# Kernel tuning notes

Hardware: AMD Instinct MI355X
Metric: run time of the kernel (lower is better)

## Reference

```python
import jax, jax.numpy as jnp
import numpy as np

B, LC, LX, LH = 2048, 20, 20, 200
D, H, V, DENSE = 128, 512, 100000, 256
MAXSEQ = 200


def _ln(x, g, b, eps=1e-5):
    m = jnp.mean(x, axis=-1, keepdims=True)
    v = jnp.mean((x - m) ** 2, axis=-1, keepdims=True)
    return (x - m) * jax.lax.rsqrt(v + eps) * g + b


def _masked_mean(x, mask):
    # x: [B,L,D], mask: [B,L] (0/1)
    m = mask.astype(x.dtype)[..., None]
    s = jnp.sum(x * m, axis=1)
    cnt = jnp.clip(jnp.sum(m, axis=1), 1.0, None)
    return s / cnt


def setup_inputs() -> dict:
    key = jax.random.key(0)
    ks = jax.random.split(key, 40)
    s = 0.02
    rn = lambda k, shape: jax.random.normal(k, shape, dtype=jnp.float32) * s
    tok_emb = rn(ks[10], (V, D)).at[0].set(0.0)          # padding_idx=0
    grp_emb = rn(ks[12], (4, D)).at[0].set(0.0)          # padding_idx=0
    return {
        'candidate_tokens': jax.random.randint(ks[0], (B, LC), 0, V),
        'context_tokens': jax.random.randint(ks[1], (B, LX), 0, V),
        'history_tokens': jax.random.randint(ks[2], (B, LH), 0, V),
        'history_positions': jax.random.randint(ks[3], (B, LH), 0, MAXSEQ + 1),
        'history_groups': jax.random.randint(ks[4], (B, LH), 0, 4),
        'candidate_mask': jax.random.randint(ks[5], (B, LC), 0, 2),
        'context_mask': jax.random.randint(ks[6], (B, LX), 0, 2),
        'history_mask': jax.random.randint(ks[7], (B, LH), 0, 2),
        'history_times': jax.random.uniform(ks[8], (B, LH), dtype=jnp.float32),
        'dense_features': jax.random.normal(ks[9], (B, DENSE), dtype=jnp.float32),
        'tok_emb': tok_emb,
        'pos_emb': rn(ks[11], (MAXSEQ + 1, D)),
        'grp_emb': grp_emb,
        'time_w1': rn(ks[13], (1, D)), 'time_b1': jnp.zeros((D,)),
        'time_w2': rn(ks[14], (D, D)), 'time_b2': jnp.zeros((D,)),
        'comp_w': rn(ks[15], (2 * D, D)), 'comp_b': jnp.zeros((D,)),
        'comp_g': jnp.ones((D,)), 'comp_bt': jnp.zeros((D,)),
        'dense_w': rn(ks[16], (DENSE, H)), 'dense_b': jnp.zeros((H,)),
        'dense_g': jnp.ones((H,)), 'dense_bt': jnp.zeros((H,)),
        'query_w': rn(ks[17], (3 * D + H, D)), 'query_b': jnp.zeros((D,)),
        'query_g': jnp.ones((D,)), 'query_bt': jnp.zeros((D,)),
        'out_w1': rn(ks[18], (7 * D + H, H)), 'out_b1': jnp.zeros((H,)),
        'out_g': jnp.ones((H,)), 'out_bt': jnp.zeros((H,)),
        'out_w2': rn(ks[19], (H, H // 2)), 'out_b2': jnp.zeros((H // 2,)),
        'out_w3': rn(ks[20], (H // 2, 1)), 'out_b3': jnp.zeros((1,)),
    }


def reference(candidate_tokens, context_tokens, history_tokens, history_positions,
              history_groups, candidate_mask, context_mask, history_mask,
              history_times, dense_features,
              tok_emb, pos_emb, grp_emb,
              time_w1, time_b1, time_w2, time_b2,
              comp_w, comp_b, comp_g, comp_bt,
              dense_w, dense_b, dense_g, dense_bt,
              query_w, query_b, query_g, query_bt,
              out_w1, out_b1, out_g, out_bt,
              out_w2, out_b2, out_w3, out_b3):
    silu = jax.nn.silu
    cand_e = tok_emb[candidate_tokens]          # [B,LC,D]
    ctx_e = tok_emb[context_tokens]             # [B,LX,D]
    tok_h = tok_emb[history_tokens]             # [B,LH,D]
    pos_h = pos_emb[history_positions]
    grp_h = grp_emb[history_groups]
    t = history_times[..., None]                # [B,LH,1]
    time_h = silu(t @ time_w1 + time_b1) @ time_w2 + time_b2
    history_embeddings = tok_h + pos_h + grp_h + time_h
    comp_in = jnp.concatenate([grp_h, time_h], axis=-1)  # [B,LH,2D]
    component_summary = silu(_ln(comp_in @ comp_w + comp_b, comp_g, comp_bt))
    cand_s = _masked_mean(cand_e, candidate_mask)
    ctx_s = _masked_mean(ctx_e, context_mask)
    comp_hist_s = _masked_mean(component_summary, history_mask)
    dense_s = silu(_ln(dense_features @ dense_w + dense_b, dense_g, dense_bt))
    q_in = jnp.concatenate([cand_s, ctx_s, comp_hist_s, dense_s], axis=-1)
    query = silu(_ln(q_in @ query_w + query_b, query_g, query_bt))  # [B,D]
    # masked attention pooling
    scores = jnp.einsum('bld,bd->bl', history_embeddings, query) / jnp.sqrt(jnp.float32(D))
    scores = jnp.where(history_mask > 0, scores, -1e9)
    attn = jax.nn.softmax(scores, axis=-1)
    hist_s = jnp.einsum('bl,bld->bd', attn, history_embeddings)
    interaction = cand_s * hist_s
    comp_inter = cand_s * comp_hist_s
    diff = jnp.abs(hist_s - comp_hist_s)
    fused = jnp.concatenate([cand_s, ctx_s, hist_s, comp_hist_s,
                             interaction, comp_inter, diff, dense_s], axis=-1)
    h1 = silu(_ln(fused @ out_w1 + out_b1, out_g, out_bt))
    h2 = silu(h1 @ out_w2 + out_b2)
    return (h2 @ out_w3 + out_b3).squeeze(-1)   # [B]
```

## Files before the change

kernel.cpp:

```cpp
#include <hip/hip_runtime.h>
#include <hip/hip_bf16.h>

#define B_ 2048
#define LC_ 20
#define LX_ 20
#define LH_ 200
#define D_ 128
#define H_ 512
#define DENSE_ 256

typedef __attribute__((ext_vector_type(8))) short short8v;
typedef __attribute__((ext_vector_type(4))) short short4v;
typedef __attribute__((ext_vector_type(4))) float floatx4;

__device__ __forceinline__ float siluf(float x) { return x / (1.f + __expf(-x)); }

__device__ __forceinline__ unsigned short f2bf(float f) {
  return __builtin_bit_cast(unsigned short, __float2bfloat16(f));
}
__device__ __forceinline__ float bf2f(unsigned short u) {
  return __bfloat162float(__builtin_bit_cast(__hip_bfloat16, u));
}

__device__ __forceinline__ float wredsum(float v) {
#pragma unroll
  for (int off = 32; off > 0; off >>= 1) v += __shfl_xor(v, off, 64);
  return v;
}

__device__ __forceinline__ int cidx(int a, int b) {
  if (a > b) { int t = a; a = b; b = t; }
  const int base[5] = {0, 5, 9, 12, 14};
  return base[a] + (b - a);
}

__global__ __launch_bounds__(128) void k0a_E(
    const float* __restrict__ w1, const float* __restrict__ b1,
    const float* __restrict__ W2, const float* __restrict__ b2,
    float* __restrict__ E) {
  __shared__ float sc[128];
  int j = threadIdx.x, p = blockIdx.x;
  {
    float w = w1[j], bb = b1[j];
    float y0 = siluf(bb);
    float y1 = siluf(0.25f * w + bb);
    float y2 = siluf(0.50f * w + bb);
    float y3 = siluf(0.75f * w + bb);
    float y4 = siluf(w + bb);
    float d1 = y1 - y0;
    float d2 = y2 - 2.f * y1 + y0;
    float d3 = y3 - 3.f * y2 + 3.f * y1 - y0;
    float d4 = y4 - 4.f * y3 + 6.f * y2 - 4.f * y1 + y0;
    float c0 = y0;
    float c1 = d1 - 0.5f * d2 + d3 * (1.f / 3.f) - 0.25f * d4;
    float c2 = 0.5f * d2 - 0.5f * d3 + (11.f / 24.f) * d4;
    float c3 = d3 * (1.f / 6.f) - 0.25f * d4;
    float c4 = d4 * (1.f / 24.f);
    float cp;
    if (p == 0) cp = c0;
    else if (p == 1) cp = c1 * 4.f;
    else if (p == 2) cp = c2 * 16.f;
    else if (p == 3) cp = c3 * 64.f;
    else cp = c4 * 256.f;
    sc[j] = cp;
  }
  __syncthreads();
  float acc = 0.f;
#pragma unroll 8
  for (int kk = 0; kk < 128; ++kk) acc += sc[kk] * W2[kk * 128 + j];
  if (p == 0) acc += b2[j];
  E[p * 128 + j] = acc;
}

__global__ __launch_bounds__(128) void k0b_FG(
    const float* __restrict__ E, const float* __restrict__ grp_emb,
    const float* __restrict__ comp_w, const float* __restrict__ comp_b,
    float* __restrict__ F, float* __restrict__ gvec) {
  __shared__ float sv[128];
  int j = threadIdx.x, blk = blockIdx.x;
  if (blk < 5) {
    sv[j] = E[blk * 128 + j];
    __syncthreads();
    float acc = 0.f;
#pragma unroll 8
    for (int kk = 0; kk < 128; ++kk) acc += sv[kk] * comp_w[(128 + kk) * 128 + j];
    if (blk == 0) acc += comp_b[j];
    F[blk * 128 + j] = acc;
  } else {
    int g = blk - 5;
    sv[j] = grp_emb[g * 128 + j];
    __syncthreads();
    float acc = 0.f;
#pragma unroll 8
    for (int kk = 0; kk < 128; ++kk) acc += sv[kk] * comp_w[kk * 128 + j];
    gvec[g * 128 + j] = acc;
  }
}

__global__ __launch_bounds__(512) void k0c_fit(
    const float* __restrict__ F, const float* __restrict__ gvec,
    const float* __restrict__ cg_, const float* __restrict__ cbt_,
    float* __restrict__ CC) {
  __shared__ float sF2[640];
  __shared__ float sGv[512];
  __shared__ float s48[48];
  __shared__ float sMC[20], sVC[36];
  int tid = threadIdx.x;
  for (int idx = tid; idx < 640; idx += 512) sF2[idx] = F[idx];
  if (tid < 512) sGv[tid] = gvec[tid];
  __syncthreads();
  int wv = tid >> 6, lane = tid & 63;
#pragma unroll
  for (int i = 0; i < 6; ++i) {
    int m = wv * 6 + i;
    if (m < 48) {
      const float* va;
      const float* vb = nullptr;
      int t = m;
      if (t < 5) va = &sF2[t * 128];
      else if (t < 9) va = &sGv[(t - 5) * 128];
      else if (t < 13) { va = &sGv[(t - 9) * 128]; vb = va; }
      else if (t < 33) {
        int g = (t - 13) / 5, p = (t - 13) % 5;
        va = &sGv[g * 128]; vb = &sF2[p * 128];
      } else {
        int idx = t - 33;
        int a = 0;
        if (idx >= 14) a = 4;
        else if (idx >= 12) a = 3;
        else if (idx >= 9) a = 2;
        else if (idx >= 5) a = 1;
        const int base[5] = {0, 5, 9, 12, 14};
        int bcol = a + (idx - base[a]);
        va = &sF2[a * 128]; vb = &sF2[bcol * 128];
      }
      float s;
      if (vb) s = va[lane] * vb[lane] + va[lane + 64] * vb[lane + 64];
      else    s = va[lane] + va[lane + 64];
      s = wredsum(s);
      if (lane == 0) s48[m] = s * (1.f / 128.f);
    }
  }
  __syncthreads();
  if (tid < 20) {
    int g = tid / 5, p = tid % 5;
    sMC[g * 5 + p] = s48[p] + (p == 0 ? s48[5 + g] : 0.f);
  }
  if (tid < 36) {
    int g = tid / 9, kk = tid % 9;
    float v = (kk == 0 ? s48[9 + g] : 0.f);
    if (kk < 5) v += 2.f * s48[13 + g * 5 + kk];
#pragma unroll
    for (int p = 0; p < 5; ++p) {
      int q = kk - p;
      if (q >= 0 && q <= 4) v += s48[33 + cidx(p, q)];
    }
    sVC[g * 9 + kk] = v;
  }
  __syncthreads();
  const float nodes[11] = {0.f, 0.02447174185f, 0.09549150281f, 0.2061073739f,
                           0.3454915028f, 0.5f, 0.6545084972f, 0.7938926261f,
                           0.9045084972f, 0.9755282581f, 1.f};
  int g = tid >> 7, j = tid & 127;
  float cgj = cg_[j], btj = cbt_[j];
  float F0 = sF2[j], F1 = sF2[128 + j], F2v = sF2[256 + j], F3 = sF2[384 + j], F4 = sF2[512 + j];
  const float* mc = &sMC[g * 5];
  const float* vc = &sVC[g * 9];
  float gv = sGv[g * 128 + j];
  float fv[11];
#pragma unroll
  for (int n = 0; n < 11; ++n) {
    float t = nodes[n];
    float mean = (((mc[4] * t + mc[3]) * t + mc[2]) * t + mc[1]) * t + mc[0];
    float e2 = vc[8];
#pragma unroll
    for (int p = 7; p >= 0; --p) e2 = e2 * t + vc[p];
    float rstd = rsqrtf(e2 - mean * mean + 1e-5f);
    float pre = gv + ((((F4 * t + F3) * t + F2v) * t + F1) * t + F0);
    fv[n] = siluf((pre - mean) * rstd * cgj + btj);
  }
#pragma unroll
  for (int ord = 1; ord <= 10; ++ord) {
#pragma unroll
    for (int n = 10; n >= 1; --n) {
      if (n >= ord) fv[n] = (fv[n] - fv[n - 1]) / (nodes[n] - nodes[n - ord]);
    }
  }
  float c[11];
#pragma unroll
  for (int i = 0; i < 11; ++i) c[i] = 0.f;
  c[0] = fv[10];
#pragma unroll
  for (int n = 9; n >= 0; --n) {
    int deg = 9 - n;
    float x = nodes[n];
    c[deg + 1] = c[deg];
#pragma unroll
    for (int i = 10; i >= 1; --i) {
      if (i <= deg) c[i] = c[i - 1] - x * c[i];
    }
    c[0] = fv[n] - x * c[0];
  }
#pragma unroll
  for (int p = 0; p < 11; ++p) CC[(g * 11 + p) * 128 + j] = c[p];
}

__global__ __launch_bounds__(256) void k_convw1t(
    const float* __restrict__ ow1, unsigned short* __restrict__ BT) {
  __shared__ float tile[64][65];
  int bk = blockIdx.x % 22;
  int bn = blockIdx.x / 22;
  int tx = threadIdx.x & 63, ty = threadIdx.x >> 6;
#pragma unroll
  for (int r = 0; r < 16; ++r) {
    int kl = ty * 16 + r;
    tile[kl][tx] = ow1[(size_t)(bk * 64 + kl) * 512 + bn * 64 + tx];
  }
  __syncthreads();
#pragma unroll
  for (int r = 0; r < 16; ++r) {
    int nl = ty * 16 + r;
    BT[(size_t)(bn * 64 + nl) * 1408 + bk * 64 + tx] = f2bf(tile[tx][nl]);
  }
}

__global__ __launch_bounds__(256) void k_convmisc(
    const float* __restrict__ ow2, const float* __restrict__ qw,
    const float* __restrict__ dw, const float* __restrict__ df,
    unsigned short* __restrict__ OW2BT, unsigned short* __restrict__ QWBT,
    unsigned short* __restrict__ DWBT, unsigned short* __restrict__ DB) {
  int idx = blockIdx.x * 256 + threadIdx.x;
  if (idx < 131072) {
    int n = idx >> 9, k = idx & 511;
    OW2BT[(size_t)n * 512 + k] = f2bf(ow2[(size_t)k * 256 + n]);
  } else if (idx < 245760) {
    int i = idx - 131072;
    int n = i / 896, k = i - n * 896;
    QWBT[(size_t)n * 896 + k] = f2bf(qw[(size_t)k * 128 + n]);
  } else if (idx < 376832) {
    int i = idx - 245760;
    int n = i >> 8, k = i & 255;
    DWBT[(size_t)n * 256 + k] = f2bf(dw[(size_t)k * 512 + n]);
  } else {
    int i = idx - 376832;
    DB[i] = f2bf(df[i]);
  }
}

__global__ __launch_bounds__(256) void k_candctx(
    const int* __restrict__ ctok, const int* __restrict__ xtok,
    const int* __restrict__ cmask, const int* __restrict__ xmask,
    const float* __restrict__ tok_emb, unsigned short* __restrict__ FB) {
  int b = blockIdx.x, tid = threadIdx.x;
  int j = tid & 127, half = tid >> 7;
  float acc = 0.f, cnt = 0.f;
  if (half == 0) {
#pragma unroll
    for (int l = 0; l < LC_; ++l) {
      float mv = (float)cmask[b * LC_ + l];
      acc += mv * tok_emb[(size_t)ctok[b * LC_ + l] * 128 + j];
      cnt += mv;
    }
    FB[(size_t)b * 1408 + j] = f2bf(acc / fmaxf(cnt, 1.f));
  } else {
#pragma unroll
    for (int l = 0; l < LX_; ++l) {
      float mv = (float)xmask[b * LX_ + l];
      acc += mv * tok_emb[(size_t)xtok[b * LX_ + l] * 128 + j];
      cnt += mv;
    }
    FB[(size_t)b * 1408 + 128 + j] = f2bf(acc / fmaxf(cnt, 1.f));
  }
}

__global__ __launch_bounds__(256) void k_comp_pow(
    const float* __restrict__ times, const int* __restrict__ groups,
    const int* __restrict__ hmask, const float* __restrict__ CC,
    unsigned short* __restrict__ FB) {
  __shared__ float sPow[LH_ * 11];
  __shared__ int sg[LH_];
  __shared__ float sS[4 * 44];
  __shared__ float sSf[44];
  int tid = threadIdx.x, b = blockIdx.x;
  if (tid < LH_) {
    float t = times[b * LH_ + tid];
    int mk = hmask[b * LH_ + tid];
    sg[tid] = mk ? groups[b * LH_ + tid] : -1;
    float pw = 1.f;
#pragma unroll
    for (int p = 0; p < 11; ++p) { sPow[tid * 11 + p] = pw; pw *= t; }
  }
  __syncthreads();
  int lane = tid & 63, w = tid >> 6;
  if (lane < 44) {
    int g = lane / 11, p = lane - 11 * g;
    float s = 0.f;
    for (int l = w * 50; l < w * 50 + 50; ++l) {
      if (sg[l] == g) s += sPow[l * 11 + p];
    }
    sS[w * 44 + lane] = s;
  }
  __syncthreads();
  if (tid < 44) sSf[tid] = sS[tid] + sS[44 + tid] + sS[88 + tid] + sS[132 + tid];
  __syncthreads();
  if (tid < 128) {
    float cnt = sSf[0] + sSf[11] + sSf[22] + sSf[33];
    float inv = 1.f / fmaxf(cnt, 1.f);
    float acc = 0.f;
#pragma unroll 4
    for (int q = 0; q < 44; ++q) acc += sSf[q] * CC[q * 128 + tid];
    FB[(size_t)b * 1408 + 384 + tid] = f2bf(acc * inv);
  }
}

__global__ __launch_bounds__(256) void k_dln(
    const unsigned short* __restrict__ A, const unsigned short* __restrict__ BT,
    const float* __restrict__ dbias, const float* __restrict__ dg,
    const float* __restrict__ dbt, unsigned short* __restrict__ FB) {
  __shared__ float sS1[64], sS2[64];
  __shared__ float sMean[16], sRstd[16];
  int tid = threadIdx.x;
  int b0 = blockIdx.x * 16;
  int w = tid >> 6, lane = tid & 63;
  int m = lane & 15, quad = lane >> 4;
  const unsigned short* ap = A + (size_t)(b0 + m) * 256 + quad * 8;
  floatx4 acc[8];
#pragma unroll
  for (int nt = 0; nt < 8; ++nt) acc[nt] = {0.f, 0.f, 0.f, 0.f};
#pragma unroll
  for (int kc = 0; kc < 256; kc += 32) {
    short8v af = *(const short8v*)&ap[kc];
#pragma unroll
    for (int nt = 0; nt < 8; ++nt) {
      const unsigned short* bp = BT + (size_t)(w * 128 + nt * 16 + m) * 256 + quad * 8;
      short8v bf = *(const short8v*)&bp[kc];
      acc[nt] = __builtin_amdgcn_mfma_f32_16x16x32_bf16(af, bf, acc[nt], 0, 0, 0);
    }
  }
  float x[8][4];
  float bi[8], gj[8], tj[8];
#pragma unroll
  for (int nt = 0; nt < 8; ++nt) {
    int col = w * 128 + nt * 16 + m;
    bi[nt] = dbias[col];
  }
  float p1[4], p2[4];
#pragma unroll
  for (int r = 0; r < 4; ++r) { p1[r] = 0.f; p2[r] = 0.f; }
#pragma unroll
  for (int nt = 0; nt < 8; ++nt) {
#pragma unroll
    for (int r = 0; r < 4; ++r) {
      float v = acc[nt][r] + bi[nt];
      x[nt][r] = v;
      p1[r] += v;
      p2[r] += v * v;
    }
  }
#pragma unroll
  for (int r = 0; r < 4; ++r) {
#pragma unroll
    for (int off = 1; off < 16; off <<= 1) {
      p1[r] += __shfl_xor(p1[r], off, 64);
      p2[r] += __shfl_xor(p2[r], off, 64);
    }
    if (m == 0) {
      sS1[(quad * 4 + r) * 4 + w] = p1[r];
      sS2[(quad * 4 + r) * 4 + w] = p2[r];
    }
  }
  __syncthreads();
  if (tid < 16) {
    float s1 = sS1[tid * 4] + sS1[tid * 4 + 1] + sS1[tid * 4 + 2] + sS1[tid * 4 + 3];
    float s2 = sS2[tid * 4] + sS2[tid * 4 + 1] + sS2[tid * 4 + 2] + sS2[tid * 4 + 3];
    float mean = s1 / 512.f, var = s2 / 512.f - mean * mean;
    sMean[tid] = mean;
    sRstd[tid] = rsqrtf(var + 1e-5f);
  }
  __syncthreads();
#pragma unroll
  for (int nt = 0; nt < 8; ++nt) {
    int col = w * 128 + nt * 16 + m;
    gj[nt] = dg[col];
    tj[nt] = dbt[col];
  }
#pragma unroll
  for (int nt = 0; nt < 8; ++nt) {
    int col = w * 128 + nt * 16 + m;
#pragma unroll
    for (int r = 0; r < 4; ++r) {
      int row16 = quad * 4 + r;
      float y = siluf((x[nt][r] - sMean[row16]) * sRstd[row16] * gj[nt] + tj[nt]);
      FB[(size_t)(b0 + row16) * 1408 + 896 + col] = f2bf(y);
    }
  }
}

__global__ __launch_bounds__(256) void k_query_mfma(
    const unsigned short* __restrict__ FB, const unsigned short* __restrict__ QWBT,
    const float* __restrict__ qb, const float* __restrict__ qg,
    const float* __restrict__ qbt, float* __restrict__ query) {
  int tid = threadIdx.x;
  int w = tid >> 6, lane = tid & 63;
  int m = lane & 15, quad = lane >> 4;
  const unsigned short* ap = FB + (size_t)(blockIdx.x * 64 + w * 16 + m) * 1408 + quad * 8;
  const unsigned short* bp = QWBT + (size_t)m * 896 + quad * 8;
  floatx4 acc[8];
#pragma unroll
  for (int nt = 0; nt < 8; ++nt) acc[nt] = {0.f, 0.f, 0.f, 0.f};
#pragma unroll 4
  for (int kc = 0; kc < 28; ++kc) {
    int fo = (kc < 8) ? kc * 32 : (kc < 12 ? 384 + (kc - 8) * 32 : 896 + (kc - 12) * 32);
    short8v af = *(const short8v*)&ap[fo];
#pragma unroll
    for (int nt = 0; nt < 8; ++nt) {
      short8v bf = *(const short8v*)&bp[(size_t)nt * 16 * 896 + kc * 32];
      acc[nt] = __builtin_amdgcn_mfma_f32_16x16x32_bf16(af, bf, acc[nt], 0, 0, 0);
    }
  }
  float bj[8], gj[8], tj[8];
#pragma unroll
  for (int nt = 0; nt < 8; ++nt) {
    bj[nt] = qb[nt * 16 + m];
    gj[nt] = qg[nt * 16 + m];
    tj[nt] = qbt[nt * 16 + m];
  }
#pragma unroll
  for (int r = 0; r < 4; ++r) {
    float x[8];
    float s1 = 0.f, s2 = 0.f;
#pragma unroll
    for (int nt = 0; nt < 8; ++nt) {
      x[nt] = acc[nt][r] + bj[nt];
      s1 += x[nt];
      s2 += x[nt] * x[nt];
    }
#pragma unroll
    for (int off = 1; off < 16; off <<= 1) {
      s1 += __shfl_xor(s1, off, 64);
      s2 += __shfl_xor(s2, off, 64);
    }
    float mean = s1 * (1.f / 128.f);
    float var = s2 * (1.f / 128.f) - mean * mean;
    float rstd = rsqrtf(var + 1e-5f);
    int row = blockIdx.x * 64 + w * 16 + quad * 4 + r;
#pragma unroll
    for (int nt = 0; nt < 8; ++nt) {
      query[(size_t)row * 128 + nt * 16 + m] = siluf((x[nt] - mean) * rstd * gj[nt] + tj[nt]);
    }
  }
}

__global__ __launch_bounds__(256) void k_attn4(
    const int* __restrict__ htok, const int* __restrict__ hpos,
    const int* __restrict__ hgrp, const int* __restrict__ hmask,
    const float* __restrict__ times,
    const float* __restrict__ tok_emb, const float* __restrict__ pos_emb,
    const float* __restrict__ grp_emb,
    const float* __restrict__ query, const float* __restrict__ E,
    unsigned short* __restrict__ FB) {
  __shared__ float sq[128];
  __shared__ float sE[5 * 128];
  __shared__ float sG[4 * 128];
  __shared__ float st[LH_];
  __shared__ float spoly[LH_];
  __shared__ int stok[LH_], spos[LH_], sgrp[LH_], smk[LH_];
  __shared__ float seq[5 * 2];
  __shared__ float s_eq[5];
  __shared__ float sA[16 * 128];
  __shared__ float sL[16];
  __shared__ float sM[16 * 5];
  int tid = threadIdx.x, b = blockIdx.x;
  int lane = tid & 63, w = tid >> 6;
  int rg = lane >> 4, li = lane & 15;
  int grp16 = w * 4 + rg;
  if (tid < 128) sq[tid] = query[b * 128 + tid];
  for (int idx = tid; idx < 5 * 128; idx += 256) sE[idx] = E[idx];
  for (int idx = tid; idx < 4 * 128; idx += 256) sG[idx] = grp_emb[idx];
  for (int l = tid; l < LH_; l += 256) {
    st[l] = times[b * LH_ + l];
    stok[l] = htok[b * LH_ + l];
    spos[l] = hpos[b * LH_ + l];
    sgrp[l] = hgrp[b * LH_ + l];
    smk[l] = hmask[b * LH_ + l];
  }
  __syncthreads();
  if (tid < 128) {
    int wh = (tid >> 6) & 1;
#pragma unroll
    for (int p = 0; p < 5; ++p) {
      float v = sE[p * 128 + tid] * sq[tid];
      v = wredsum(v);
      if ((tid & 63) == 0) seq[p * 2 + wh] = v;
    }
  }
  __syncthreads();
  if (tid < 5) s_eq[tid] = seq[tid * 2] + seq[tid * 2 + 1];
  __syncthreads();
  if (tid < LH_) {
    float t = st[tid];
    spoly[tid] = (((s_eq[4] * t + s_eq[3]) * t + s_eq[2]) * t + s_eq[1]) * t + s_eq[0];
  }
  __syncthreads();
  const float4 qa = *(const float4*)&sq[li * 8];
  const float4 qb4 = *(const float4*)&sq[li * 8 + 4];
  const float scale = 0.08838834764831845f;
  float a0 = 0.f, a1 = 0.f, a2 = 0.f, a3 = 0.f, a4 = 0.f, a5 = 0.f, a6 = 0.f, a7 = 0.f;
  float lsum = 0.f, mom1 = 0.f, mom2 = 0.f, mom3 = 0.f, mom4 = 0.f;
  for (int l = grp16; l < LH_; l += 16) {
    if (smk[l]) {
      int tok = stok[l], pos = spos[l], g = sgrp[l];
      const float* tp_ = &tok_emb[(size_t)tok * 128 + li * 8];
      const float* pp_ = &pos_emb[pos * 128 + li * 8];
      float4 ta = *(const float4*)tp_;
      float4 tb = *(const float4*)(tp_ + 4);
      float4 pa = *(const float4*)pp_;
      float4 pb = *(const float4*)(pp_ + 4);
      const float* gp_ = &sG[g * 128 + li * 8];
      float4 ga = *(const float4*)gp_;
      float4 gb = *(const float4*)(gp_ + 4);
      float v0 = ta.x + pa.x + ga.x, v1 = ta.y + pa.y + ga.y;
      float v2 = ta.z + pa.z + ga.z, v3 = ta.w + pa.w + ga.w;
      float v4 = tb.x + pb.x + gb.x, v5 = tb.y + pb.y + gb.y;
      float v6 = tb.z + pb.z + gb.z, v7 = tb.w + pb.w + gb.w;
      float d = v0 * qa.x + v1 * qa.y + v2 * qa.z + v3 * qa.w +
                v4 * qb4.x + v5 * qb4.y + v6 * qb4.z + v7 * qb4.w;
      d += __shfl_xor(d, 1, 64);
      d += __shfl_xor(d, 2, 64);
      d += __shfl_xor(d, 4, 64);
      d += __shfl_xor(d, 8, 64);
      float e = __expf((d + spoly[l]) * scale);
      float t = st[l];
      lsum += e;
      a0 += e * v0; a1 += e * v1; a2 += e * v2; a3 += e * v3;
      a4 += e * v4; a5 += e * v5; a6 += e * v6; a7 += e * v7;
      float tp = e * t;
      mom1 += tp; tp *= t;
      mom2 += tp; tp *= t;
      mom3 += tp; tp *= t;
      mom4 += tp;
    }
  }
  float* ap2 = &sA[grp16 * 128 + li * 8];
  ap2[0] = a0; ap2[1] = a1; ap2[2] = a2; ap2[3] = a3;
  ap2[4] = a4; ap2[5] = a5; ap2[6] = a6; ap2[7] = a7;
  if (li == 0) {
    sL[grp16] = lsum;
    sM[grp16 * 5 + 1] = mom1; sM[grp16 * 5 + 2] = mom2;
    sM[grp16 * 5 + 3] = mom3; sM[grp16 * 5 + 4] = mom4;
  }
  __syncthreads();
  if (tid < 128) {
    int i = tid;
    float L = 0.f;
#pragma unroll
    for (int k = 0; k < 16; ++k) L += sL[k];
    float inv = 1.f / L;
    float v = 0.f;
#pragma unroll
    for (int k = 0; k < 16; ++k) v += sA[k * 128 + i];
    v *= inv;
    v += sE[i];
#pragma unroll
    for (int p = 1; p < 5; ++p) {
      float mp = 0.f;
#pragma unroll
      for (int k = 0; k < 16; ++k) mp += sM[k * 5 + p];
      v += mp * inv * sE[p * 128 + i];
    }
    unsigned short* row = FB + (size_t)b * 1408;
    float c = bf2f(row[i]), cm = bf2f(row[384 + i]);
    row[256 + i] = f2bf(v);
    row[512 + i] = f2bf(c * v);
    row[640 + i] = f2bf(c * cm);
    row[768 + i] = f2bf(fabsf(v - cm));
  }
}

__global__ __launch_bounds__(256) void k_gemm1(
    const unsigned short* __restrict__ A, const unsigned short* __restrict__ BT,
    float* __restrict__ H1) {
  int tid = threadIdx.x;
  int bm = blockIdx.x >> 3;
  int bn = blockIdx.x & 7;
  int w = tid >> 6, lane = tid & 63;
  int m = lane & 15, quad = lane >> 4;
  const unsigned short* ap = A + (size_t)(bm * 64 + w * 16 + m) * 1408 + quad * 8;
  const unsigned short* bp0 = BT + (size_t)(bn * 64 + m) * 1408 + quad * 8;
  const unsigned short* bp1 = bp0 + 16 * 1408;
  const unsigned short* bp2 = bp0 + 32 * 1408;
  const unsigned short* bp3 = bp0 + 48 * 1408;
  floatx4 acc0 = {0.f, 0.f, 0.f, 0.f};
  floatx4 acc1 = {0.f, 0.f, 0.f, 0.f};
  floatx4 acc2 = {0.f, 0.f, 0.f, 0.f};
  floatx4 acc3 = {0.f, 0.f, 0.f, 0.f};
#pragma unroll 4
  for (int kc = 0; kc < 1408; kc += 32) {
    short8v af = *(const short8v*)&ap[kc];
    short8v b0 = *(const short8v*)&bp0[kc];
    short8v b1 = *(const short8v*)&bp1[kc];
    short8v b2 = *(const short8v*)&bp2[kc];
    short8v b3 = *(const short8v*)&bp3[kc];
    acc0 = __builtin_amdgcn_mfma_f32_16x16x32_bf16(af, b0, acc0, 0, 0, 0);
    acc1 = __builtin_amdgcn_mfma_f32_16x16x32_bf16(af, b1, acc1, 0, 0, 0);
    acc2 = __builtin_amdgcn_mfma_f32_16x16x32_bf16(af, b2, acc2, 0, 0, 0);
    acc3 = __builtin_amdgcn_mfma_f32_16x16x32_bf16(af, b3, acc3, 0, 0, 0);
  }
  int row = bm * 64 + w * 16 + quad * 4;
  int col = bn * 64 + m;
#pragma unroll
  for (int r = 0; r < 4; ++r) {
    H1[(size_t)(row + r) * 512 + col] = acc0[r];
    H1[(size_t)(row + r) * 512 + col + 16] = acc1[r];
    H1[(size_t)(row + r) * 512 + col + 32] = acc2[r];
    H1[(size_t)(row + r) * 512 + col + 48] = acc3[r];
  }
}

__global__ __launch_bounds__(256) void k_ep2(
    const float* __restrict__ H1, const float* __restrict__ ob1,
    const float* __restrict__ og, const float* __restrict__ obt,
    const unsigned short* __restrict__ OW2BT, const float* __restrict__ ob2,
    const float* __restrict__ ow3, const float* __restrict__ ob3,
    float* __restrict__ out) {
  __shared__ short sB[16 * 520];
  __shared__ float sD[64];
  int tid = threadIdx.x;
  int b0 = blockIdx.x * 16;
  {
    int g = tid >> 4, li = tid & 15;
    const float* hrow = H1 + (size_t)(b0 + g) * 512;
    float4 xv[8];
    float s1 = 0.f, s2 = 0.f;
#pragma unroll
    for (int k = 0; k < 8; ++k) {
      int col = li * 4 + k * 64;
      float4 v = *(const float4*)&hrow[col];
      float4 bb = *(const float4*)&ob1[col];
      v.x += bb.x; v.y += bb.y; v.z += bb.z; v.w += bb.w;
      xv[k] = v;
      s1 += v.x + v.y + v.z + v.w;
      s2 += v.x * v.x + v.y * v.y + v.z * v.z + v.w * v.w;
    }
#pragma unroll
    for (int off = 1; off < 16; off <<= 1) {
      s1 += __shfl_xor(s1, off, 64);
      s2 += __shfl_xor(s2, off, 64);
    }
    float mean = s1 * (1.f / 512.f);
    float var = s2 * (1.f / 512.f) - mean * mean;
    float rstd = rsqrtf(var + 1e-5f);
#pragma unroll
    for (int k = 0; k < 8; ++k) {
      int col = li * 4 + k * 64;
      float4 gg = *(const float4*)&og[col];
      float4 tt = *(const float4*)&obt[col];
      short4v pk;
      pk.x = (short)f2bf(siluf((xv[k].x - mean) * rstd * gg.x + tt.x));
      pk.y = (short)f2bf(siluf((xv[k].y - mean) * rstd * gg.y + tt.y));
      pk.z = (short)f2bf(siluf((xv[k].z - mean) * rstd * gg.z + tt.z));
      pk.w = (short)f2bf(siluf((xv[k].w - mean) * rstd * gg.w + tt.w));
      *(short4v*)((char*)sB + g * 1040 + li * 8 + k * 128) = pk;
    }
  }
  __syncthreads();
  int w = tid >> 6, lane = tid & 63;
  int m = lane & 15, quad = lane >> 4;
  floatx4 acc[4];
#pragma unroll
  for (int nt = 0; nt < 4; ++nt) acc[nt] = {0.f, 0.f, 0.f, 0.f};
#pragma unroll
  for (int kc = 0; kc < 16; ++kc) {
    short8v af = *(const short8v*)((const char*)sB + m * 1040 + quad * 16 + kc * 64);
#pragma unroll
    for (int nt = 0; nt < 4; ++nt) {
      const unsigned short* bp = OW2BT + (size_t)(w * 64 + nt * 16 + m) * 512 + quad * 8;
      short8v bf = *(const short8v*)&bp[kc * 32];
      acc[nt] = __builtin_amdgcn_mfma_f32_16x16x32_bf16(af, bf, acc[nt], 0, 0, 0);
    }
  }
  float pz[4];
#pragma unroll
  for (int r = 0; r < 4; ++r) pz[r] = 0.f;
#pragma unroll
  for (int nt = 0; nt < 4; ++nt) {
    int col = w * 64 + nt * 16 + m;
    float c2 = ob2[col], w3 = ow3[col];
#pragma unroll
    for (int r = 0; r < 4; ++r) pz[r] += siluf(acc[nt][r] + c2) * w3;
  }
#pragma unroll
  for (int r = 0; r < 4; ++r) {
#pragma unroll
    for (int off = 1; off < 16; off <<= 1) pz[r] += __shfl_xor(pz[r], off, 64);
    if (m == 0) sD[(quad * 4 + r) * 4 + w] = pz[r];
  }
  __syncthreads();
  if (tid < 16) {
    out[b0 + tid] = sD[tid * 4] + sD[tid * 4 + 1] + sD[tid * 4 + 2] + sD[tid * 4 + 3] + ob3[0];
  }
}

extern "C" void kernel_launch(void* const* d_in, const int* in_sizes, int n_in,
                              void* d_out, int out_size, void* d_ws, size_t ws_size,
                              hipStream_t stream) {
  const int* cand_tok = (const int*)d_in[0];
  const int* ctx_tok = (const int*)d_in[1];
  const int* hist_tok = (const int*)d_in[2];
  const int* hist_pos = (const int*)d_in[3];
  const int* hist_grp = (const int*)d_in[4];
  const int* cand_mask = (const int*)d_in[5];
  const int* ctx_mask = (const int*)d_in[6];
  const int* hist_mask = (const int*)d_in[7];
  const float* hist_times = (const float*)d_in[8];
  const float* dense_feat = (const float*)d_in[9];
  const float* tok_emb = (const float*)d_in[10];
  const float* pos_emb = (const float*)d_in[11];
  const float* grp_emb = (const float*)d_in[12];
  const float* time_w1 = (const float*)d_in[13];
  const float* time_b1 = (const float*)d_in[14];
  const float* time_w2 = (const float*)d_in[15];
  const float* time_b2 = (const float*)d_in[16];
  const float* comp_w = (const float*)d_in[17];
  const float* comp_b = (const float*)d_in[18];
  const float* comp_g = (const float*)d_in[19];
  const float* comp_bt = (const float*)d_in[20];
  const float* dense_w = (const float*)d_in[21];
  const float* dense_b = (const float*)d_in[22];
  const float* dense_g = (const float*)d_in[23];
  const float* dense_bt = (const float*)d_in[24];
  const float* query_w = (const float*)d_in[25];
  const float* query_b = (const float*)d_in[26];
  const float* query_g = (const float*)d_in[27];
  const float* query_bt = (const float*)d_in[28];
  const float* out_w1 = (const float*)d_in[29];
  const float* out_b1 = (const float*)d_in[30];
  const float* out_g = (const float*)d_in[31];
  const float* out_bt = (const float*)d_in[32];
  const float* out_w2 = (const float*)d_in[33];
  const float* out_b2 = (const float*)d_in[34];
  const float* out_w3 = (const float*)d_in[35];
  const float* out_b3 = (const float*)d_in[36];
  float* out = (float*)d_out;

  float* ws = (float*)d_ws;
  float* E = ws;
  float* CC = ws + 640;
  float* Fs = ws + 6272;
  float* gvecs = ws + 6912;
  float* query = ws + 8192;
  unsigned short* OW2BT = (unsigned short*)(ws + 1318912);
  unsigned short* QWBT = (unsigned short*)(ws + 1384448);
  unsigned short* DWBT = (unsigned short*)(ws + 1441792);
  unsigned short* DB = (unsigned short*)(ws + 1507328);
  float* H1 = ws + 2099200;
  unsigned short* FB = (unsigned short*)(ws + 3147776);
  unsigned short* OW1BT = (unsigned short*)(ws + 4589568);

  k0a_E<<<5, 128, 0, stream>>>(time_w1, time_b1, time_w2, time_b2, E);
  k0b_FG<<<9, 128, 0, stream>>>(E, grp_emb, comp_w, comp_b, Fs, gvecs);
  k0c_fit<<<1, 512, 0, stream>>>(Fs, gvecs, comp_g, comp_bt, CC);
  k_convw1t<<<176, 256, 0, stream>>>(out_w1, OW1BT);
  k_convmisc<<<3520, 256, 0, stream>>>(out_w2, query_w, dense_w, dense_feat,
                                       OW2BT, QWBT, DWBT, DB);
  k_candctx<<<B_, 256, 0, stream>>>(cand_tok, ctx_tok, cand_mask, ctx_mask,
                                    tok_emb, FB);
  k_comp_pow<<<B_, 256, 0, stream>>>(hist_times, hist_grp, hist_mask, CC, FB);
  k_dln<<<B_ / 16, 256, 0, stream>>>(DB, DWBT, dense_b, dense_g, dense_bt, FB);
  k_query_mfma<<<32, 256, 0, stream>>>(FB, QWBT, query_b, query_g, query_bt, query);
  k_attn4<<<B_, 256, 0, stream>>>(hist_tok, hist_pos, hist_grp, hist_mask, hist_times,
                                  tok_emb, pos_emb, grp_emb, query, E, FB);
  k_gemm1<<<256, 256, 0, stream>>>(FB, OW1BT, H1);
  k_ep2<<<B_ / 16, 256, 0, stream>>>(H1, out_b1, out_g, out_bt,
                                     OW2BT, out_b2, out_w3, out_b3, out);
}
```

Measured before the change: 311.3 us.

## Split query GEMM K-dimension across warps and launch 128 blocks

The query projection kernel previously used 32 blocks, each warp owning 16 rows and the full K loop. Now each block handles 16 rows, with the four warps each taking a quarter of the K chunks. Partial sums are reduced through shared memory before the LayerNorm and SiLU epilogue. This raises the grid to 128 blocks to fill more of the GPU, at the cost of a shared-memory reduction, a barrier, and four times more reads of the weight matrix across blocks.

```diff
diff --git a/kernel.cpp b/kernel.cpp
--- a/kernel.cpp
+++ b/kernel.cpp
@@ -400,16 +400,19 @@
     const unsigned short* __restrict__ FB, const unsigned short* __restrict__ QWBT,
     const float* __restrict__ qb, const float* __restrict__ qg,
     const float* __restrict__ qbt, float* __restrict__ query) {
+  __shared__ float sP[4][16][128];
   int tid = threadIdx.x;
+  int b0 = blockIdx.x * 16;
   int w = tid >> 6, lane = tid & 63;
   int m = lane & 15, quad = lane >> 4;
-  const unsigned short* ap = FB + (size_t)(blockIdx.x * 64 + w * 16 + m) * 1408 + quad * 8;
+  const unsigned short* ap = FB + (size_t)(b0 + m) * 1408 + quad * 8;
   const unsigned short* bp = QWBT + (size_t)m * 896 + quad * 8;
   floatx4 acc[8];
 #pragma unroll
   for (int nt = 0; nt < 8; ++nt) acc[nt] = {0.f, 0.f, 0.f, 0.f};
-#pragma unroll 4
-  for (int kc = 0; kc < 28; ++kc) {
+#pragma unroll
+  for (int ki = 0; ki < 7; ++ki) {
+    int kc = w + ki * 4;
     int fo = (kc < 8) ? kc * 32 : (kc < 12 ? 384 + (kc - 8) * 32 : 896 + (kc - 12) * 32);
     short8v af = *(const short8v*)&ap[fo];
 #pragma unroll
@@ -418,36 +421,37 @@
       acc[nt] = __builtin_amdgcn_mfma_f32_16x16x32_bf16(af, bf, acc[nt], 0, 0, 0);
     }
   }
-  float bj[8], gj[8], tj[8];
 #pragma unroll
   for (int nt = 0; nt < 8; ++nt) {
-    bj[nt] = qb[nt * 16 + m];
-    gj[nt] = qg[nt * 16 + m];
-    tj[nt] = qbt[nt * 16 + m];
-  }
-#pragma unroll
-  for (int r = 0; r < 4; ++r) {
-    float x[8];
-    float s1 = 0.f, s2 = 0.f;
-#pragma unroll
-    for (int nt = 0; nt < 8; ++nt) {
-      x[nt] = acc[nt][r] + bj[nt];
-      s1 += x[nt];
-      s2 += x[nt] * x[nt];
-    }
-#pragma unroll
-    for (int off = 1; off < 16; off <<= 1) {
-      s1 += __shfl_xor(s1, off, 64);
-      s2 += __shfl_xor(s2, off, 64);
-    }
-    float mean = s1 * (1.f / 128.f);
-    float var = s2 * (1.f / 128.f) - mean * mean;
-    float rstd = rsqrtf(var + 1e-5f);
-    int row = blockIdx.x * 64 + w * 16 + quad * 4 + r;
-#pragma unroll
-    for (int nt = 0; nt < 8; ++nt) {
-      query[(size_t)row * 128 + nt * 16 + m] = siluf((x[nt] - mean) * rstd * gj[nt] + tj[nt]);
-    }
+#pragma unroll
+    for (int r = 0; r < 4; ++r) {
+      sP[w][quad * 4 + r][nt * 16 + m] = acc[nt][r];
+    }
+  }
+  __syncthreads();
+  int row = tid >> 4, cb = (tid & 15) * 8;
+  float x[8];
+  float s1 = 0.f, s2 = 0.f;
+#pragma unroll
+  for (int j = 0; j < 8; ++j) {
+    int c = cb + j;
+    float v = sP[0][row][c] + sP[1][row][c] + sP[2][row][c] + sP[3][row][c] + qb[c];
+    x[j] = v;
+    s1 += v;
+    s2 += v * v;
+  }
+#pragma unroll
+  for (int off = 1; off < 16; off <<= 1) {
+    s1 += __shfl_xor(s1, off, 64);
+    s2 += __shfl_xor(s2, off, 64);
+  }
+  float mean = s1 * (1.f / 128.f);
+  float var = s2 * (1.f / 128.f) - mean * mean;
+  float rstd = rsqrtf(var + 1e-5f);
+#pragma unroll
+  for (int j = 0; j < 8; ++j) {
+    int c = cb + j;
+    query[(size_t)(b0 + row) * 128 + c] = siluf((x[j] - mean) * rstd * qg[c] + qbt[c]);
   }
 }
 
@@ -767,7 +771,7 @@
                                     tok_emb, FB);
   k_comp_pow<<<B_, 256, 0, stream>>>(hist_times, hist_grp, hist_mask, CC, FB);
   k_dln<<<B_ / 16, 256, 0, stream>>>(DB, DWBT, dense_b, dense_g, dense_bt, FB);
-  k_query_mfma<<<32, 256, 0, stream>>>(FB, QWBT, query_b, query_g, query_bt, query);
+  k_query_mfma<<<B_ / 16, 256, 0, stream>>>(FB, QWBT, query_b, query_g, query_bt, query);
   k_attn4<<<B_, 256, 0, stream>>>(hist_tok, hist_pos, hist_grp, hist_mask, hist_times,
                                   tok_emb, pos_emb, grp_emb, query, E, FB);
   k_gemm1<<<256, 256, 0, stream>>>(FB, OW1BT, H1);
```

Measured after the change: 283.8 us. -8.8%, faster.
